# Performance work log

Measured on AMD Instinct MI355X. Metric: run time of the kernel, lower is better.

## Reference

```python
import jax, jax.numpy as jnp
import numpy as np

D, H, E, K, S = 1024, 2048, 8, 2, 1  # dim, expert hidden, n_experts, top_k, n_shared
B, L = 4, 2048


def setup_inputs() -> dict:
    key = jax.random.key(0)
    ks = jax.random.split(key, 9)
    std = 0.02
    return {
        "x": jax.random.normal(ks[0], (B, L, D), dtype=jnp.float32),
        "router_w": jax.random.normal(ks[1], (E, D), dtype=jnp.float32) * std,
        "experts_bias": jnp.zeros((E,), dtype=jnp.float32),  # aux-free LB bias buffer
        "w1": jax.random.normal(ks[2], (E, D, H), dtype=jnp.float32) * std,
        "w3": jax.random.normal(ks[3], (E, D, H), dtype=jnp.float32) * std,
        "w2": jax.random.normal(ks[4], (E, H, D), dtype=jnp.float32) * std,
        "sw1": jax.random.normal(ks[5], (S, D, H), dtype=jnp.float32) * std,
        "sw3": jax.random.normal(ks[6], (S, D, H), dtype=jnp.float32) * std,
        "sw2": jax.random.normal(ks[7], (S, H, D), dtype=jnp.float32) * std,
    }


def reference(x, router_w, experts_bias, w1, w3, w2, sw1, sw3, sw2):
    b, l, d = x.shape
    xf = x.reshape(-1, d)  # [T, D], T = b*l

    # shared experts (SwiGLU FFN), summed over S
    sg = jnp.einsum("td,sdh->tsh", xf, sw1)
    su = jnp.einsum("td,sdh->tsh", xf, sw3)
    shared_out = jnp.einsum("tsh,shd->td", jax.nn.silu(sg) * su, sw2)

    # router + aux-free load-balancing bias
    logits = xf @ router_w.T + experts_bias  # [T, E]
    rw, sel = jax.lax.top_k(logits, K)       # [T, K]
    rw = jax.nn.softmax(rw.astype(jnp.float32), axis=-1).astype(x.dtype)

    # combine weights scattered to [T, E]; equals torch one_hot dispatch+index_add
    cw = (jax.nn.one_hot(sel, E, dtype=x.dtype) * rw[..., None]).sum(axis=1)

    # all-expert SwiGLU, weighted-combined (identical math: unselected weight = 0)
    g = jnp.einsum("td,edh->teh", xf, w1)
    u = jnp.einsum("td,edh->teh", xf, w3)
    eo = jax.nn.silu(g) * u  # [T, E, H]
    moe_out = jnp.einsum("te,teh,ehd->td", cw, eo, w2)

    return (moe_out + shared_out).reshape(b, l, d)
```

## Files before the change

kernel.cpp:

```cpp
#include <hip/hip_runtime.h>
#include <stdint.h>

#define T_TOK 8192
#define DIMV  1024
#define HIDV  2048
#define NE    8
#define CAP   8192
#define ROUTED 16384
#define ASSIGN_TOT 24576

typedef __attribute__((ext_vector_type(8))) short          bf16x8;
typedef __attribute__((ext_vector_type(8))) unsigned short u16x8;
typedef __attribute__((ext_vector_type(4))) float          floatx4;

__device__ __forceinline__ unsigned short f2bf(float f) {
    union { float f; unsigned int i; } v; v.f = f;
    unsigned int i = v.i;
    return (unsigned short)((i + 0x7FFFu + ((i >> 16) & 1u)) >> 16);
}
__device__ __forceinline__ float bf2f(unsigned short u) {
    union { unsigned int i; float f; } v; v.i = ((unsigned int)u) << 16; return v.f;
}

__device__ __forceinline__ void gll16(const void* g, void* l) {
    __builtin_amdgcn_global_load_lds((const __attribute__((address_space(1))) void*)g,
                                     (__attribute__((address_space(3))) void*)l,
                                     16, 0, 0);
}

__global__ __launch_bounds__(256) void router_kernel(
    const float* __restrict__ x,
    const float* __restrict__ rwp,
    const float* __restrict__ biasp,
    unsigned short* __restrict__ xb,
    int* __restrict__ cnt, int* __restrict__ tlist,
    int* __restrict__ pos, float* __restrict__ pw)
{
    const int t    = blockIdx.x * 4 + (threadIdx.x >> 6);
    const int lane = threadIdx.x & 63;
    const float* xr = x + (size_t)t * DIMV + lane * 16;
    float xf[16];
#pragma unroll
    for (int q = 0; q < 4; q++) {
        float4 v = *(const float4*)(xr + q * 4);
        xf[q*4+0] = v.x; xf[q*4+1] = v.y; xf[q*4+2] = v.z; xf[q*4+3] = v.w;
    }
    {
        u16x8 o0, o1;
#pragma unroll
        for (int j = 0; j < 8; j++) { o0[j] = f2bf(xf[j]); o1[j] = f2bf(xf[8 + j]); }
        unsigned short* xo = xb + (size_t)t * DIMV + lane * 16;
        *(u16x8*)xo = o0;
        *(u16x8*)(xo + 8) = o1;
    }
    float acc[NE];
#pragma unroll
    for (int e = 0; e < NE; e++) {
        const float* wr = rwp + (size_t)e * DIMV + lane * 16;
        float s = 0.f;
#pragma unroll
        for (int q = 0; q < 4; q++) {
            float4 v = *(const float4*)(wr + q * 4);
            s += xf[q*4+0]*v.x + xf[q*4+1]*v.y + xf[q*4+2]*v.z + xf[q*4+3]*v.w;
        }
        acc[e] = s;
    }
#pragma unroll
    for (int e = 0; e < NE; e++)
#pragma unroll
        for (int off = 32; off; off >>= 1) acc[e] += __shfl_xor(acc[e], off, 64);

    if (lane == 0) {
        float lg[NE];
#pragma unroll
        for (int e = 0; e < NE; e++) lg[e] = acc[e] + biasp[e];
        int e0 = 0;
#pragma unroll
        for (int e = 1; e < NE; e++) if (lg[e] > lg[e0]) e0 = e;
        int e1 = (e0 == 0) ? 1 : 0;
#pragma unroll
        for (int e = 0; e < NE; e++) if (e != e0 && lg[e] > lg[e1]) e1 = e;
        float z  = __expf(lg[e1] - lg[e0]);
        float p0 = 1.f / (1.f + z);
        float p1 = z  / (1.f + z);
        int s0 = atomicAdd(cnt + e0, 1);
        tlist[e0 * CAP + s0] = t;
        int s1 = atomicAdd(cnt + e1, 1);
        tlist[e1 * CAP + s1] = t;
        pos[2 * t + 0] = e0 * CAP + s0;
        pos[2 * t + 1] = e1 * CAP + s1;
        pw[2 * t + 0] = p0;
        pw[2 * t + 1] = p1;
    }
}

template<int R, int C>
__device__ __forceinline__ void ctrans_body(
    const float* __restrict__ src, unsigned short* __restrict__ dstp,
    unsigned short (*tile)[66])
{
    const int c0 = blockIdx.x * 64, r0 = blockIdx.y * 64;
    const int tid = threadIdx.x;
    const int lr = tid >> 4;
    const int lc = (tid & 15) * 4;
#pragma unroll
    for (int i = 0; i < 4; i++) {
        int r = lr + 16 * i;
        float4 v = *(const float4*)(src + (size_t)(r0 + r) * C + (c0 + lc));
        ushort4 o; o.x = f2bf(v.x); o.y = f2bf(v.y); o.z = f2bf(v.z); o.w = f2bf(v.w);
        *(ushort4*)&tile[r][lc] = o;
    }
    __syncthreads();
    const int oc  = tid >> 3;
    const int orr = (tid & 7) * 8;
#pragma unroll
    for (int i = 0; i < 2; i++) {
        int c = oc + 32 * i;
        u16x8 tmp;
#pragma unroll
        for (int j = 0; j < 8; j++) tmp[j] = tile[orr + j][c];
        *(u16x8*)(dstp + (size_t)(c0 + c) * R + (r0 + orr)) = tmp;
    }
}

__global__ __launch_bounds__(256) void ctrans_all(
    const float* __restrict__ w1, const float* __restrict__ w3,
    const float* __restrict__ sw1, const float* __restrict__ sw3,
    const float* __restrict__ w2, const float* __restrict__ sw2,
    unsigned short* __restrict__ w1t, unsigned short* __restrict__ w3t,
    unsigned short* __restrict__ sw1t, unsigned short* __restrict__ sw3t,
    unsigned short* __restrict__ w2t, unsigned short* __restrict__ sw2t)
{
    __shared__ unsigned short tile[64][66];
    const int z = blockIdx.z;
    if (z < 18) {
        if (blockIdx.y >= DIMV / 64) return;
        const float* src; unsigned short* dstp;
        if (z < 8)        { src = w1 + (size_t)z * DIMV * HIDV;       dstp = w1t + (size_t)z * DIMV * HIDV; }
        else if (z < 16)  { src = w3 + (size_t)(z - 8) * DIMV * HIDV; dstp = w3t + (size_t)(z - 8) * DIMV * HIDV; }
        else if (z == 16) { src = sw1; dstp = sw1t; }
        else              { src = sw3; dstp = sw3t; }
        ctrans_body<DIMV, HIDV>(src, dstp, tile);
    } else {
        if (blockIdx.x >= DIMV / 64) return;
        const float* src; unsigned short* dstp;
        if (z < 26) { src = w2 + (size_t)(z - 18) * HIDV * DIMV; dstp = w2t + (size_t)(z - 18) * HIDV * DIMV; }
        else        { src = sw2; dstp = sw2t; }
        ctrans_body<HIDV, DIMV>(src, dstp, tile);
    }
}

__global__ __launch_bounds__(256, 2) void up_gemm(
    const unsigned short* __restrict__ x,
    const unsigned short* __restrict__ w1t,
    const unsigned short* __restrict__ w3t,
    const unsigned short* __restrict__ sw1t,
    const unsigned short* __restrict__ sw3t,
    const int* __restrict__ cnt, const int* __restrict__ tlist,
    unsigned short* __restrict__ hbuf)
{
    const int g = blockIdx.z;
    int n_rows, row_off;
    const unsigned short *B1p, *B3p;
    if (g < NE) {
        row_off = 0;
        for (int e = 0; e < g; e++) row_off += cnt[e];
        n_rows = cnt[g];
        B1p = w1t + (size_t)g * HIDV * DIMV;
        B3p = w3t + (size_t)g * HIDV * DIMV;
    } else {
        n_rows = T_TOK; row_off = ROUTED;
        B1p = sw1t; B3p = sw3t;
    }
    const int m0 = blockIdx.y * 128;
    if (m0 >= n_rows) return;
    const int n0 = blockIdx.x * 64;

    __shared__ __align__(16) unsigned short Al[128 * 32];
    __shared__ __align__(16) unsigned short B1l[64 * 32];
    __shared__ __align__(16) unsigned short B3l[64 * 32];

    const int tid  = threadIdx.x;
    const int lane = tid & 63;
    const int wave = tid >> 6;
    const int r0   = tid >> 2;
    const int ck   = (tid & 3) ^ ((r0 >> 1) & 3);

    int tokA, tokB;
    if (g < NE) {
        int ra = m0 + r0, rb = m0 + 64 + r0;
        tokA = (ra < n_rows) ? tlist[g * CAP + ra] : 0;
        tokB = (rb < n_rows) ? tlist[g * CAP + rb] : 0;
    } else { tokA = m0 + r0; tokB = m0 + 64 + r0; }

    const unsigned short* gA0 = x + (size_t)tokA * DIMV + ck * 8;
    const unsigned short* gA1 = x + (size_t)tokB * DIMV + ck * 8;
    const unsigned short* gB1 = B1p + (size_t)(n0 + r0) * DIMV + ck * 8;
    const unsigned short* gB3 = B3p + (size_t)(n0 + r0) * DIMV + ck * 8;

    char* AlB0 = (char*)Al  + wave * 1024;
    char* AlB1 = (char*)Al  + 4096 + wave * 1024;
    char* B1B  = (char*)B1l + wave * 1024;
    char* B3B  = (char*)B3l + wave * 1024;

    const int wm = wave & 1, wn = wave >> 1;
    const int m16 = lane & 15, quad = lane >> 4;
    const int sw  = (m16 >> 1) & 3;

    floatx4 accg[4][2] = {};
    floatx4 accu[4][2] = {};

    const unsigned short* Afp  = Al  + (wm * 64 + m16) * 32 + (quad ^ sw) * 8;
    const unsigned short* B1fp = B1l + (wn * 32 + m16) * 32 + (quad ^ sw) * 8;
    const unsigned short* B3fp = B3l + (wn * 32 + m16) * 32 + (quad ^ sw) * 8;

    for (int k0 = 0; k0 < DIMV; k0 += 32) {
        __syncthreads();
        gll16(gA0 + k0, AlB0);
        gll16(gA1 + k0, AlB1);
        gll16(gB1 + k0, B1B);
        gll16(gB3 + k0, B3B);
        __syncthreads();
        bf16x8 af[4], b1f[2], b3f[2];
#pragma unroll
        for (int i = 0; i < 4; i++) af[i] = *(const bf16x8*)(Afp + i * 16 * 32);
#pragma unroll
        for (int j = 0; j < 2; j++) {
            b1f[j] = *(const bf16x8*)(B1fp + j * 16 * 32);
            b3f[j] = *(const bf16x8*)(B3fp + j * 16 * 32);
        }
#pragma unroll
        for (int i = 0; i < 4; i++)
#pragma unroll
            for (int j = 0; j < 2; j++) {
                accg[i][j] = __builtin_amdgcn_mfma_f32_16x16x32_bf16(af[i], b1f[j], accg[i][j], 0, 0, 0);
                accu[i][j] = __builtin_amdgcn_mfma_f32_16x16x32_bf16(af[i], b3f[j], accu[i][j], 0, 0, 0);
            }
    }

#pragma unroll
    for (int i = 0; i < 4; i++) {
#pragma unroll
        for (int ii = 0; ii < 4; ii++) {
            int r = m0 + wm * 64 + i * 16 + quad * 4 + ii;
            if (r < n_rows) {
#pragma unroll
                for (int j = 0; j < 2; j++) {
                    int col = n0 + wn * 32 + j * 16 + m16;
                    float gv = accg[i][j][ii], uv = accu[i][j][ii];
                    float s  = gv / (1.0f + __expf(-gv));
                    hbuf[(size_t)(row_off + r) * HIDV + col] = f2bf(s * uv);
                }
            }
        }
    }
}

__global__ __launch_bounds__(256, 2) void down_gemm(
    const unsigned short* __restrict__ hbuf,
    const unsigned short* __restrict__ w2t,
    const unsigned short* __restrict__ sw2t,
    const int* __restrict__ cnt,
    unsigned short* __restrict__ dbuf)
{
    const int g = blockIdx.z;
    int n_rows, row_off;
    const unsigned short* Bp;
    if (g < NE) {
        row_off = 0;
        for (int e = 0; e < g; e++) row_off += cnt[e];
        n_rows = cnt[g];
        Bp = w2t + (size_t)g * DIMV * HIDV;
    } else {
        n_rows = T_TOK; row_off = ROUTED;
        Bp = sw2t;
    }
    const int m0 = blockIdx.y * 128;
    if (m0 >= n_rows) return;
    const int n0 = blockIdx.x * 128;

    __shared__ __align__(16) unsigned short Al[128 * 32];
    __shared__ __align__(16) unsigned short Bl[128 * 32];

    const int tid  = threadIdx.x;
    const int lane = tid & 63;
    const int wave = tid >> 6;
    const int r0   = tid >> 2;
    const int ck   = (tid & 3) ^ ((r0 >> 1) & 3);

    const unsigned short* gA0 = hbuf + (size_t)(row_off + m0 + r0) * HIDV + ck * 8;
    const unsigned short* gA1 = gA0 + (size_t)64 * HIDV;
    const unsigned short* gB0 = Bp + (size_t)(n0 + r0) * HIDV + ck * 8;
    const unsigned short* gB1 = gB0 + (size_t)64 * HIDV;

    char* AlB0 = (char*)Al + wave * 1024;
    char* AlB1 = (char*)Al + 4096 + wave * 1024;
    char* BB0  = (char*)Bl + wave * 1024;
    char* BB1  = (char*)Bl + 4096 + wave * 1024;

    const int wm = wave & 1, wn = wave >> 1;
    const int m16 = lane & 15, quad = lane >> 4;
    const int sw  = (m16 >> 1) & 3;

    floatx4 acc[4][4] = {};

    const unsigned short* Afp = Al + (wm * 64 + m16) * 32 + (quad ^ sw) * 8;
    const unsigned short* Bfp = Bl + (wn * 64 + m16) * 32 + (quad ^ sw) * 8;

    for (int k0 = 0; k0 < HIDV; k0 += 32) {
        __syncthreads();
        gll16(gA0 + k0, AlB0);
        gll16(gA1 + k0, AlB1);
        gll16(gB0 + k0, BB0);
        gll16(gB1 + k0, BB1);
        __syncthreads();
        bf16x8 af[4], bf[4];
#pragma unroll
        for (int i = 0; i < 4; i++) af[i] = *(const bf16x8*)(Afp + i * 16 * 32);
#pragma unroll
        for (int j = 0; j < 4; j++) bf[j] = *(const bf16x8*)(Bfp + j * 16 * 32);
#pragma unroll
        for (int i = 0; i < 4; i++)
#pragma unroll
            for (int j = 0; j < 4; j++)
                acc[i][j] = __builtin_amdgcn_mfma_f32_16x16x32_bf16(af[i], bf[j], acc[i][j], 0, 0, 0);
    }

#pragma unroll
    for (int i = 0; i < 4; i++) {
#pragma unroll
        for (int ii = 0; ii < 4; ii++) {
            int r = m0 + wm * 64 + i * 16 + quad * 4 + ii;
            if (r < n_rows) {
                unsigned short* drow = dbuf + (size_t)(row_off + r) * DIMV;
#pragma unroll
                for (int j = 0; j < 4; j++) {
                    int col = n0 + wn * 64 + j * 16 + m16;
                    drow[col] = f2bf(acc[i][j][ii]);
                }
            }
        }
    }
}

__global__ __launch_bounds__(256) void combine_kernel(
    const unsigned short* __restrict__ dbuf,
    const int* __restrict__ cnt, const int* __restrict__ pos,
    const float* __restrict__ pw, float* __restrict__ outp)
{
    const int tid = threadIdx.x;
    const int t = blockIdx.x * 2 + (tid >> 7);
    const int c = (tid & 127) * 8;
    int goff[NE];
    {
        int s = 0;
#pragma unroll
        for (int e = 0; e < NE; e++) { goff[e] = s; s += cnt[e]; }
    }
    const int p0 = pos[2 * t], p1 = pos[2 * t + 1];
    const float w0 = pw[2 * t], w1 = pw[2 * t + 1];
    const int r0 = goff[p0 >> 13] + (p0 & (CAP - 1));
    const int r1 = goff[p1 >> 13] + (p1 & (CAP - 1));
    const u16x8 v0 = *(const u16x8*)(dbuf + (size_t)r0 * DIMV + c);
    const u16x8 v1 = *(const u16x8*)(dbuf + (size_t)r1 * DIMV + c);
    const u16x8 vs = *(const u16x8*)(dbuf + (size_t)(ROUTED + t) * DIMV + c);
    float o[8];
#pragma unroll
    for (int j = 0; j < 8; j++)
        o[j] = w0 * bf2f(v0[j]) + w1 * bf2f(v1[j]) + bf2f(vs[j]);
    float* op = outp + (size_t)t * DIMV + c;
    *(float4*)op       = make_float4(o[0], o[1], o[2], o[3]);
    *(float4*)(op + 4) = make_float4(o[4], o[5], o[6], o[7]);
}

extern "C" void kernel_launch(void* const* d_in, const int* in_sizes, int n_in,
                              void* d_out, int out_size, void* d_ws, size_t ws_size,
                              hipStream_t stream)
{
    (void)in_sizes; (void)n_in; (void)out_size; (void)ws_size;
    const float* x    = (const float*)d_in[0];
    const float* rw   = (const float*)d_in[1];
    const float* bias = (const float*)d_in[2];
    const float* w1   = (const float*)d_in[3];
    const float* w3   = (const float*)d_in[4];
    const float* w2   = (const float*)d_in[5];
    const float* sw1  = (const float*)d_in[6];
    const float* sw3  = (const float*)d_in[7];
    const float* sw2  = (const float*)d_in[8];
    float* outp = (float*)d_out;

    char* p = (char*)d_ws;
    auto alloc = [&](size_t b) { char* r = p; p += (b + 255) & ~(size_t)255; return r; };
    int*   cnt   = (int*)  alloc(64);
    int*   tlist = (int*)  alloc((size_t)NE * CAP * 4);
    int*   pos   = (int*)  alloc((size_t)T_TOK * 2 * 4);
    float* pw    = (float*)alloc((size_t)T_TOK * 2 * 4);
    unsigned short* xb   = (unsigned short*)alloc((size_t)T_TOK * DIMV * 2);
    unsigned short* hbuf = (unsigned short*)alloc((size_t)ASSIGN_TOT * HIDV * 2);
    unsigned short* w1t  = (unsigned short*)alloc((size_t)NE * HIDV * DIMV * 2);
    unsigned short* w3t  = (unsigned short*)alloc((size_t)NE * HIDV * DIMV * 2);
    unsigned short* w2t  = (unsigned short*)alloc((size_t)NE * DIMV * HIDV * 2);
    unsigned short* sw1t = (unsigned short*)alloc((size_t)HIDV * DIMV * 2);
    unsigned short* sw3t = (unsigned short*)alloc((size_t)HIDV * DIMV * 2);
    unsigned short* sw2t = (unsigned short*)alloc((size_t)DIMV * HIDV * 2);
    unsigned short* dbuf = w1t;

    hipMemsetAsync(cnt, 0, 64, stream);

    dim3 blk(256);
    router_kernel<<<dim3(T_TOK/4), blk, 0, stream>>>(x, rw, bias, xb, cnt, tlist, pos, pw);
    ctrans_all<<<dim3(HIDV/64, HIDV/64, 27), blk, 0, stream>>>(w1, w3, sw1, sw3, w2, sw2,
                                                               w1t, w3t, sw1t, sw3t, w2t, sw2t);
    up_gemm<<<dim3(HIDV/64, 64, 9), blk, 0, stream>>>(xb, w1t, w3t, sw1t, sw3t,
                                                      cnt, tlist, hbuf);
    down_gemm<<<dim3(DIMV/128, 64, 9), blk, 0, stream>>>(hbuf, w2t, sw2t, cnt, dbuf);
    combine_kernel<<<dim3(T_TOK/2), blk, 0, stream>>>(dbuf, cnt, pos, pw, outp);
}
```

Measured before the change: 858.3 us.

## Rewrite up/down GEMMs as 256x256-tile, 8-wave, double-buffered pipelined kernels with interleaved w1/w3

The weight transpose now interleaves w1 and w3 rows in 16-row groups into one concatenated matrix, so the up GEMM becomes a single GEMM with gate/up pairs side by side. Both expert GEMMs move to 512-thread blocks with 256x256 output tiles and 128 KB dynamic LDS, double-buffered so global-to-LDS loads for upcoming k-steps overlap the MFMA work. The loop uses explicit waitcnt, barrier and setprio scheduling. This aims for more data reuse per LDS byte and better latency hiding. The cost is much larger tiles, which waste more work on partially filled expert tiles and allow fewer blocks per CU. Relying on 128 KB of dynamic shared memory also assumes the launch supports that size.

```diff
diff --git a/kernel.cpp b/kernel.cpp
--- a/kernel.cpp
+++ b/kernel.cpp
@@ -8,6 +8,7 @@
 #define CAP   8192
 #define ROUTED 16384
 #define ASSIGN_TOT 24576
+#define NCAT  4096
 
 typedef __attribute__((ext_vector_type(8))) short          bf16x8;
 typedef __attribute__((ext_vector_type(8))) unsigned short u16x8;
@@ -97,7 +98,7 @@
 template<int R, int C>
 __device__ __forceinline__ void ctrans_body(
     const float* __restrict__ src, unsigned short* __restrict__ dstp,
-    unsigned short (*tile)[66])
+    unsigned short (*tile)[66], int ileave, int ubit)
 {
     const int c0 = blockIdx.x * 64, r0 = blockIdx.y * 64;
     const int tid = threadIdx.x;
@@ -116,10 +117,12 @@
 #pragma unroll
     for (int i = 0; i < 2; i++) {
         int c = oc + 32 * i;
+        int h = c0 + c;
+        int row = ileave ? (((h >> 4) << 5) + ubit * 16 + (h & 15)) : h;
         u16x8 tmp;
 #pragma unroll
         for (int j = 0; j < 8; j++) tmp[j] = tile[orr + j][c];
-        *(u16x8*)(dstp + (size_t)(c0 + c) * R + (r0 + orr)) = tmp;
+        *(u16x8*)(dstp + (size_t)row * R + (r0 + orr)) = tmp;
     }
 }
 
@@ -127,136 +130,180 @@
     const float* __restrict__ w1, const float* __restrict__ w3,
     const float* __restrict__ sw1, const float* __restrict__ sw3,
     const float* __restrict__ w2, const float* __restrict__ sw2,
-    unsigned short* __restrict__ w1t, unsigned short* __restrict__ w3t,
-    unsigned short* __restrict__ sw1t, unsigned short* __restrict__ sw3t,
+    unsigned short* __restrict__ wcat, unsigned short* __restrict__ scat,
     unsigned short* __restrict__ w2t, unsigned short* __restrict__ sw2t)
 {
     __shared__ unsigned short tile[64][66];
     const int z = blockIdx.z;
     if (z < 18) {
         if (blockIdx.y >= DIMV / 64) return;
-        const float* src; unsigned short* dstp;
-        if (z < 8)        { src = w1 + (size_t)z * DIMV * HIDV;       dstp = w1t + (size_t)z * DIMV * HIDV; }
-        else if (z < 16)  { src = w3 + (size_t)(z - 8) * DIMV * HIDV; dstp = w3t + (size_t)(z - 8) * DIMV * HIDV; }
-        else if (z == 16) { src = sw1; dstp = sw1t; }
-        else              { src = sw3; dstp = sw3t; }
-        ctrans_body<DIMV, HIDV>(src, dstp, tile);
+        const float* src; unsigned short* dstp; int u;
+        if (z < 8)        { src = w1 + (size_t)z * DIMV * HIDV;       dstp = wcat + (size_t)z * NCAT * DIMV;       u = 0; }
+        else if (z < 16)  { src = w3 + (size_t)(z - 8) * DIMV * HIDV; dstp = wcat + (size_t)(z - 8) * NCAT * DIMV; u = 1; }
+        else if (z == 16) { src = sw1; dstp = scat; u = 0; }
+        else              { src = sw3; dstp = scat; u = 1; }
+        ctrans_body<DIMV, HIDV>(src, dstp, tile, 1, u);
     } else {
         if (blockIdx.x >= DIMV / 64) return;
         const float* src; unsigned short* dstp;
-        if (z < 26) { src = w2 + (size_t)(z - 18) * HIDV * DIMV; dstp = w2t + (size_t)(z - 18) * HIDV * DIMV; }
+        if (z < 26) { src = w2 + (size_t)(z - 18) * HIDV * DIMV; dstp = w2t + (size_t)(z - 18) * DIMV * HIDV; }
         else        { src = sw2; dstp = sw2t; }
-        ctrans_body<HIDV, DIMV>(src, dstp, tile);
-    }
-}
-
-__global__ __launch_bounds__(256, 2) void up_gemm(
+        ctrans_body<HIDV, DIMV>(src, dstp, tile, 0, 0);
+    }
+}
+
+
+__global__ __launch_bounds__(512, 2) void up_gemm8(
     const unsigned short* __restrict__ x,
-    const unsigned short* __restrict__ w1t,
-    const unsigned short* __restrict__ w3t,
-    const unsigned short* __restrict__ sw1t,
-    const unsigned short* __restrict__ sw3t,
+    const unsigned short* __restrict__ wcat,
+    const unsigned short* __restrict__ scat,
     const int* __restrict__ cnt, const int* __restrict__ tlist,
     unsigned short* __restrict__ hbuf)
 {
     const int g = blockIdx.z;
-    int n_rows, row_off;
-    const unsigned short *B1p, *B3p;
+    int n_rows, row_off = 0;
+    const unsigned short* Bp;
     if (g < NE) {
-        row_off = 0;
         for (int e = 0; e < g; e++) row_off += cnt[e];
         n_rows = cnt[g];
-        B1p = w1t + (size_t)g * HIDV * DIMV;
-        B3p = w3t + (size_t)g * HIDV * DIMV;
-    } else {
-        n_rows = T_TOK; row_off = ROUTED;
-        B1p = sw1t; B3p = sw3t;
-    }
-    const int m0 = blockIdx.y * 128;
+        Bp = wcat + (size_t)g * NCAT * DIMV;
+    } else { n_rows = T_TOK; row_off = ROUTED; Bp = scat; }
+    const int m0 = blockIdx.y * 256;
     if (m0 >= n_rows) return;
-    const int n0 = blockIdx.x * 64;
-
-    __shared__ __align__(16) unsigned short Al[128 * 32];
-    __shared__ __align__(16) unsigned short B1l[64 * 32];
-    __shared__ __align__(16) unsigned short B3l[64 * 32];
+    const int n0 = blockIdx.x * 256;
+
+    extern __shared__ __align__(16) unsigned short smem[];
+    unsigned short* As = smem;
+    unsigned short* Bs = smem + 32768;
 
     const int tid  = threadIdx.x;
     const int lane = tid & 63;
     const int wave = tid >> 6;
-    const int r0   = tid >> 2;
-    const int ck   = (tid & 3) ^ ((r0 >> 1) & 3);
-
-    int tokA, tokB;
+    const int wm = wave >> 2, wn = wave & 3;
+    const int m16 = lane & 15, quad = lane >> 4;
+
+    const int sr = tid >> 2;
+    const int sc = (((tid & 3) ^ (sr & 3)) << 3);
+
+    int tA0, tA1;
     if (g < NE) {
-        int ra = m0 + r0, rb = m0 + 64 + r0;
-        tokA = (ra < n_rows) ? tlist[g * CAP + ra] : 0;
-        tokB = (rb < n_rows) ? tlist[g * CAP + rb] : 0;
-    } else { tokA = m0 + r0; tokB = m0 + 64 + r0; }
-
-    const unsigned short* gA0 = x + (size_t)tokA * DIMV + ck * 8;
-    const unsigned short* gA1 = x + (size_t)tokB * DIMV + ck * 8;
-    const unsigned short* gB1 = B1p + (size_t)(n0 + r0) * DIMV + ck * 8;
-    const unsigned short* gB3 = B3p + (size_t)(n0 + r0) * DIMV + ck * 8;
-
-    char* AlB0 = (char*)Al  + wave * 1024;
-    char* AlB1 = (char*)Al  + 4096 + wave * 1024;
-    char* B1B  = (char*)B1l + wave * 1024;
-    char* B3B  = (char*)B3l + wave * 1024;
-
-    const int wm = wave & 1, wn = wave >> 1;
-    const int m16 = lane & 15, quad = lane >> 4;
-    const int sw  = (m16 >> 1) & 3;
-
-    floatx4 accg[4][2] = {};
-    floatx4 accu[4][2] = {};
-
-    const unsigned short* Afp  = Al  + (wm * 64 + m16) * 32 + (quad ^ sw) * 8;
-    const unsigned short* B1fp = B1l + (wn * 32 + m16) * 32 + (quad ^ sw) * 8;
-    const unsigned short* B3fp = B3l + (wn * 32 + m16) * 32 + (quad ^ sw) * 8;
-
-    for (int k0 = 0; k0 < DIMV; k0 += 32) {
-        __syncthreads();
-        gll16(gA0 + k0, AlB0);
-        gll16(gA1 + k0, AlB1);
-        gll16(gB1 + k0, B1B);
-        gll16(gB3 + k0, B3B);
-        __syncthreads();
-        bf16x8 af[4], b1f[2], b3f[2];
-#pragma unroll
-        for (int i = 0; i < 4; i++) af[i] = *(const bf16x8*)(Afp + i * 16 * 32);
-#pragma unroll
-        for (int j = 0; j < 2; j++) {
-            b1f[j] = *(const bf16x8*)(B1fp + j * 16 * 32);
-            b3f[j] = *(const bf16x8*)(B3fp + j * 16 * 32);
-        }
-#pragma unroll
-        for (int i = 0; i < 4; i++)
-#pragma unroll
-            for (int j = 0; j < 2; j++) {
-                accg[i][j] = __builtin_amdgcn_mfma_f32_16x16x32_bf16(af[i], b1f[j], accg[i][j], 0, 0, 0);
-                accu[i][j] = __builtin_amdgcn_mfma_f32_16x16x32_bf16(af[i], b3f[j], accu[i][j], 0, 0, 0);
-            }
-    }
-
-#pragma unroll
-    for (int i = 0; i < 4; i++) {
+        int ra = m0 + sr;       if (ra >= n_rows) ra = n_rows - 1;
+        int rb = m0 + 128 + sr; if (rb >= n_rows) rb = n_rows - 1;
+        tA0 = tlist[g * CAP + ra];
+        tA1 = tlist[g * CAP + rb];
+    } else { tA0 = m0 + sr; tA1 = m0 + 128 + sr; }
+    const unsigned short* sA0 = x + (size_t)tA0 * DIMV + sc;
+    const unsigned short* sA1 = x + (size_t)tA1 * DIMV + sc;
+    const unsigned short* sB0 = Bp + (size_t)(n0 + sr) * DIMV + sc;
+    const unsigned short* sB1 = Bp + (size_t)(n0 + 128 + sr) * DIMV + sc;
+
+    unsigned short* dA = As + wave * 512;
+    unsigned short* dB = Bs + wave * 512;
+
+#define UPSA(t, kk) { unsigned short* d_ = dA + (((t) & 1) << 14) + ((kk) << 13); \
+        gll16(sA0 + (t) * 64 + (kk) * 32, d_); gll16(sA1 + (t) * 64 + (kk) * 32, d_ + 4096); }
+#define UPSB(t, kk) { unsigned short* d_ = dB + (((t) & 1) << 14) + ((kk) << 13); \
+        gll16(sB0 + (t) * 64 + (kk) * 32, d_); gll16(sB1 + (t) * 64 + (kk) * 32, d_ + 4096); }
+
+    const unsigned short* Afb = As + (wm * 128 + m16) * 32 + ((quad ^ (m16 & 3)) << 3);
+    const unsigned short* Bfb = Bs + (wn * 64  + m16) * 32 + ((quad ^ (m16 & 3)) << 3);
+
+    UPSB(0, 0); UPSA(0, 0); UPSB(0, 1); UPSA(0, 1);
+    UPSB(1, 0); UPSA(1, 0); UPSB(1, 1);
+    asm volatile("s_waitcnt vmcnt(6)" ::: "memory");
+    __builtin_amdgcn_s_barrier();
+
+    floatx4 acc[8][4] = {};
+    bf16x8 af[4], bfr[4];
+
+#define NTU 16
+    for (int t = 0; t < NTU; ++t) {
+        const int pb = (t & 1) << 14;
+        const unsigned short* Ab = Afb + pb;
+        const unsigned short* Bb = Bfb + pb;
+#pragma unroll
+        for (int i = 0; i < 4; i++) af[i]  = *(const bf16x8*)(Ab + i * 512);
+#pragma unroll
+        for (int j = 0; j < 4; j++) bfr[j] = *(const bf16x8*)(Bb + j * 512);
+        if (t + 1 < NTU) UPSA(t + 1, 1);
+        __builtin_amdgcn_s_barrier();
+        asm volatile("s_waitcnt lgkmcnt(0)" ::: "memory");
+        __builtin_amdgcn_s_setprio(1);
+#pragma unroll
+        for (int i = 0; i < 4; i++)
+#pragma unroll
+            for (int j = 0; j < 4; j++)
+                acc[i][j] = __builtin_amdgcn_mfma_f32_16x16x32_bf16(af[i], bfr[j], acc[i][j], 0, 0, 0);
+        __builtin_amdgcn_s_setprio(0);
+        __builtin_amdgcn_s_barrier();
+#pragma unroll
+        for (int i = 0; i < 4; i++) af[i] = *(const bf16x8*)(Ab + (4 + i) * 512);
+        if (t + 2 < NTU) UPSB(t + 2, 0);
+        __builtin_amdgcn_s_barrier();
+        asm volatile("s_waitcnt lgkmcnt(0)" ::: "memory");
+        __builtin_amdgcn_s_setprio(1);
+#pragma unroll
+        for (int i = 0; i < 4; i++)
+#pragma unroll
+            for (int j = 0; j < 4; j++)
+                acc[4 + i][j] = __builtin_amdgcn_mfma_f32_16x16x32_bf16(af[i], bfr[j], acc[4 + i][j], 0, 0, 0);
+        __builtin_amdgcn_s_setprio(0);
+        __builtin_amdgcn_s_barrier();
+#pragma unroll
+        for (int i = 0; i < 4; i++) af[i]  = *(const bf16x8*)(Ab + 8192 + i * 512);
+#pragma unroll
+        for (int j = 0; j < 4; j++) bfr[j] = *(const bf16x8*)(Bb + 8192 + j * 512);
+        if (t + 2 < NTU) UPSA(t + 2, 0);
+        __builtin_amdgcn_s_barrier();
+        asm volatile("s_waitcnt lgkmcnt(0)" ::: "memory");
+        __builtin_amdgcn_s_setprio(1);
+#pragma unroll
+        for (int i = 0; i < 4; i++)
+#pragma unroll
+            for (int j = 0; j < 4; j++)
+                acc[i][j] = __builtin_amdgcn_mfma_f32_16x16x32_bf16(af[i], bfr[j], acc[i][j], 0, 0, 0);
+        __builtin_amdgcn_s_setprio(0);
+        __builtin_amdgcn_s_barrier();
+#pragma unroll
+        for (int i = 0; i < 4; i++) af[i] = *(const bf16x8*)(Ab + 8192 + (4 + i) * 512);
+        if (t + 2 < NTU) UPSB(t + 2, 1);
+        __builtin_amdgcn_s_barrier();
+        asm volatile("s_waitcnt lgkmcnt(0)" ::: "memory");
+        __builtin_amdgcn_s_setprio(1);
+#pragma unroll
+        for (int i = 0; i < 4; i++)
+#pragma unroll
+            for (int j = 0; j < 4; j++)
+                acc[4 + i][j] = __builtin_amdgcn_mfma_f32_16x16x32_bf16(af[i], bfr[j], acc[4 + i][j], 0, 0, 0);
+        __builtin_amdgcn_s_setprio(0);
+        if (t < NTU - 2) { asm volatile("s_waitcnt vmcnt(6)" ::: "memory"); }
+        else             { asm volatile("s_waitcnt vmcnt(0)" ::: "memory"); }
+        __builtin_amdgcn_s_barrier();
+    }
+#undef NTU
+#undef UPSA
+#undef UPSB
+
+    const int hb = (n0 >> 1) + wn * 32;
+#pragma unroll
+    for (int mi = 0; mi < 8; mi++) {
 #pragma unroll
         for (int ii = 0; ii < 4; ii++) {
-            int r = m0 + wm * 64 + i * 16 + quad * 4 + ii;
+            int r = m0 + wm * 128 + mi * 16 + quad * 4 + ii;
             if (r < n_rows) {
-#pragma unroll
-                for (int j = 0; j < 2; j++) {
-                    int col = n0 + wn * 32 + j * 16 + m16;
-                    float gv = accg[i][j][ii], uv = accu[i][j][ii];
+                unsigned short* hr = hbuf + (size_t)(row_off + r) * HIDV;
+#pragma unroll
+                for (int p = 0; p < 2; p++) {
+                    float gv = acc[mi][2 * p][ii], uv = acc[mi][2 * p + 1][ii];
                     float s  = gv / (1.0f + __expf(-gv));
-                    hbuf[(size_t)(row_off + r) * HIDV + col] = f2bf(s * uv);
+                    hr[hb + p * 16 + m16] = f2bf(s * uv);
                 }
             }
         }
     }
 }
 
-__global__ __launch_bounds__(256, 2) void down_gemm(
+__global__ __launch_bounds__(512, 2) void down_gemm8(
     const unsigned short* __restrict__ hbuf,
     const unsigned short* __restrict__ w2t,
     const unsigned short* __restrict__ sw2t,
@@ -264,80 +311,132 @@
     unsigned short* __restrict__ dbuf)
 {
     const int g = blockIdx.z;
-    int n_rows, row_off;
+    int n_rows, row_off = 0;
     const unsigned short* Bp;
     if (g < NE) {
-        row_off = 0;
         for (int e = 0; e < g; e++) row_off += cnt[e];
         n_rows = cnt[g];
         Bp = w2t + (size_t)g * DIMV * HIDV;
-    } else {
-        n_rows = T_TOK; row_off = ROUTED;
-        Bp = sw2t;
-    }
-    const int m0 = blockIdx.y * 128;
+    } else { n_rows = T_TOK; row_off = ROUTED; Bp = sw2t; }
+    const int m0 = blockIdx.y * 256;
     if (m0 >= n_rows) return;
-    const int n0 = blockIdx.x * 128;
-
-    __shared__ __align__(16) unsigned short Al[128 * 32];
-    __shared__ __align__(16) unsigned short Bl[128 * 32];
+    const int n0 = blockIdx.x * 256;
+
+    extern __shared__ __align__(16) unsigned short smem[];
+    unsigned short* As = smem;
+    unsigned short* Bs = smem + 32768;
 
     const int tid  = threadIdx.x;
     const int lane = tid & 63;
     const int wave = tid >> 6;
-    const int r0   = tid >> 2;
-    const int ck   = (tid & 3) ^ ((r0 >> 1) & 3);
-
-    const unsigned short* gA0 = hbuf + (size_t)(row_off + m0 + r0) * HIDV + ck * 8;
-    const unsigned short* gA1 = gA0 + (size_t)64 * HIDV;
-    const unsigned short* gB0 = Bp + (size_t)(n0 + r0) * HIDV + ck * 8;
-    const unsigned short* gB1 = gB0 + (size_t)64 * HIDV;
-
-    char* AlB0 = (char*)Al + wave * 1024;
-    char* AlB1 = (char*)Al + 4096 + wave * 1024;
-    char* BB0  = (char*)Bl + wave * 1024;
-    char* BB1  = (char*)Bl + 4096 + wave * 1024;
-
-    const int wm = wave & 1, wn = wave >> 1;
+    const int wm = wave >> 2, wn = wave & 3;
     const int m16 = lane & 15, quad = lane >> 4;
-    const int sw  = (m16 >> 1) & 3;
-
-    floatx4 acc[4][4] = {};
-
-    const unsigned short* Afp = Al + (wm * 64 + m16) * 32 + (quad ^ sw) * 8;
-    const unsigned short* Bfp = Bl + (wn * 64 + m16) * 32 + (quad ^ sw) * 8;
-
-    for (int k0 = 0; k0 < HIDV; k0 += 32) {
-        __syncthreads();
-        gll16(gA0 + k0, AlB0);
-        gll16(gA1 + k0, AlB1);
-        gll16(gB0 + k0, BB0);
-        gll16(gB1 + k0, BB1);
-        __syncthreads();
-        bf16x8 af[4], bf[4];
-#pragma unroll
-        for (int i = 0; i < 4; i++) af[i] = *(const bf16x8*)(Afp + i * 16 * 32);
-#pragma unroll
-        for (int j = 0; j < 4; j++) bf[j] = *(const bf16x8*)(Bfp + j * 16 * 32);
-#pragma unroll
-        for (int i = 0; i < 4; i++)
-#pragma unroll
-            for (int j = 0; j < 4; j++)
-                acc[i][j] = __builtin_amdgcn_mfma_f32_16x16x32_bf16(af[i], bf[j], acc[i][j], 0, 0, 0);
-    }
-
-#pragma unroll
-    for (int i = 0; i < 4; i++) {
+
+    const int sr = tid >> 2;
+    const int sc = (((tid & 3) ^ (sr & 3)) << 3);
+
+    const unsigned short* sA0 = hbuf + (size_t)(row_off + m0 + sr) * HIDV + sc;
+    const unsigned short* sA1 = sA0 + (size_t)128 * HIDV;
+    const unsigned short* sB0 = Bp + (size_t)(n0 + sr) * HIDV + sc;
+    const unsigned short* sB1 = sB0 + (size_t)128 * HIDV;
+
+    unsigned short* dA = As + wave * 512;
+    unsigned short* dB = Bs + wave * 512;
+
+#define DNSA(t, kk) { unsigned short* d_ = dA + (((t) & 1) << 14) + ((kk) << 13); \
+        gll16(sA0 + (t) * 64 + (kk) * 32, d_); gll16(sA1 + (t) * 64 + (kk) * 32, d_ + 4096); }
+#define DNSB(t, kk) { unsigned short* d_ = dB + (((t) & 1) << 14) + ((kk) << 13); \
+        gll16(sB0 + (t) * 64 + (kk) * 32, d_); gll16(sB1 + (t) * 64 + (kk) * 32, d_ + 4096); }
+
+    const unsigned short* Afb = As + (wm * 128 + m16) * 32 + ((quad ^ (m16 & 3)) << 3);
+    const unsigned short* Bfb = Bs + (wn * 64  + m16) * 32 + ((quad ^ (m16 & 3)) << 3);
+
+    DNSB(0, 0); DNSA(0, 0); DNSB(0, 1); DNSA(0, 1);
+    DNSB(1, 0); DNSA(1, 0); DNSB(1, 1);
+    asm volatile("s_waitcnt vmcnt(6)" ::: "memory");
+    __builtin_amdgcn_s_barrier();
+
+    floatx4 acc[8][4] = {};
+    bf16x8 af[4], bfr[4];
+
+#define NTD 32
+    for (int t = 0; t < NTD; ++t) {
+        const int pb = (t & 1) << 14;
+        const unsigned short* Ab = Afb + pb;
+        const unsigned short* Bb = Bfb + pb;
+#pragma unroll
+        for (int i = 0; i < 4; i++) af[i]  = *(const bf16x8*)(Ab + i * 512);
+#pragma unroll
+        for (int j = 0; j < 4; j++) bfr[j] = *(const bf16x8*)(Bb + j * 512);
+        if (t + 1 < NTD) DNSA(t + 1, 1);
+        __builtin_amdgcn_s_barrier();
+        asm volatile("s_waitcnt lgkmcnt(0)" ::: "memory");
+        __builtin_amdgcn_s_setprio(1);
+#pragma unroll
+        for (int i = 0; i < 4; i++)
+#pragma unroll
+            for (int j = 0; j < 4; j++)
+                acc[i][j] = __builtin_amdgcn_mfma_f32_16x16x32_bf16(af[i], bfr[j], acc[i][j], 0, 0, 0);
+        __builtin_amdgcn_s_setprio(0);
+        __builtin_amdgcn_s_barrier();
+#pragma unroll
+        for (int i = 0; i < 4; i++) af[i] = *(const bf16x8*)(Ab + (4 + i) * 512);
+        if (t + 2 < NTD) DNSB(t + 2, 0);
+        __builtin_amdgcn_s_barrier();
+        asm volatile("s_waitcnt lgkmcnt(0)" ::: "memory");
+        __builtin_amdgcn_s_setprio(1);
+#pragma unroll
+        for (int i = 0; i < 4; i++)
+#pragma unroll
+            for (int j = 0; j < 4; j++)
+                acc[4 + i][j] = __builtin_amdgcn_mfma_f32_16x16x32_bf16(af[i], bfr[j], acc[4 + i][j], 0, 0, 0);
+        __builtin_amdgcn_s_setprio(0);
+        __builtin_amdgcn_s_barrier();
+#pragma unroll
+        for (int i = 0; i < 4; i++) af[i]  = *(const bf16x8*)(Ab + 8192 + i * 512);
+#pragma unroll
+        for (int j = 0; j < 4; j++) bfr[j] = *(const bf16x8*)(Bb + 8192 + j * 512);
+        if (t + 2 < NTD) DNSA(t + 2, 0);
+        __builtin_amdgcn_s_barrier();
+        asm volatile("s_waitcnt lgkmcnt(0)" ::: "memory");
+        __builtin_amdgcn_s_setprio(1);
+#pragma unroll
+        for (int i = 0; i < 4; i++)
+#pragma unroll
+            for (int j = 0; j < 4; j++)
+                acc[i][j] = __builtin_amdgcn_mfma_f32_16x16x32_bf16(af[i], bfr[j], acc[i][j], 0, 0, 0);
+        __builtin_amdgcn_s_setprio(0);
+        __builtin_amdgcn_s_barrier();
+#pragma unroll
+        for (int i = 0; i < 4; i++) af[i] = *(const bf16x8*)(Ab + 8192 + (4 + i) * 512);
+        if (t + 2 < NTD) DNSB(t + 2, 1);
+        __builtin_amdgcn_s_barrier();
+        asm volatile("s_waitcnt lgkmcnt(0)" ::: "memory");
+        __builtin_amdgcn_s_setprio(1);
+#pragma unroll
+        for (int i = 0; i < 4; i++)
+#pragma unroll
+            for (int j = 0; j < 4; j++)
+                acc[4 + i][j] = __builtin_amdgcn_mfma_f32_16x16x32_bf16(af[i], bfr[j], acc[4 + i][j], 0, 0, 0);
+        __builtin_amdgcn_s_setprio(0);
+        if (t < NTD - 2) { asm volatile("s_waitcnt vmcnt(6)" ::: "memory"); }
+        else             { asm volatile("s_waitcnt vmcnt(0)" ::: "memory"); }
+        __builtin_amdgcn_s_barrier();
+    }
+#undef NTD
+#undef DNSA
+#undef DNSB
+
+#pragma unroll
+    for (int mi = 0; mi < 8; mi++) {
 #pragma unroll
         for (int ii = 0; ii < 4; ii++) {
-            int r = m0 + wm * 64 + i * 16 + quad * 4 + ii;
+            int r = m0 + wm * 128 + mi * 16 + quad * 4 + ii;
             if (r < n_rows) {
                 unsigned short* drow = dbuf + (size_t)(row_off + r) * DIMV;
 #pragma unroll
-                for (int j = 0; j < 4; j++) {
-                    int col = n0 + wn * 64 + j * 16 + m16;
-                    drow[col] = f2bf(acc[i][j][ii]);
-                }
+                for (int nj = 0; nj < 4; nj++)
+                    drow[n0 + wn * 64 + nj * 16 + m16] = f2bf(acc[mi][nj][ii]);
             }
         }
     }
@@ -397,22 +496,21 @@
     float* pw    = (float*)alloc((size_t)T_TOK * 2 * 4);
     unsigned short* xb   = (unsigned short*)alloc((size_t)T_TOK * DIMV * 2);
     unsigned short* hbuf = (unsigned short*)alloc((size_t)ASSIGN_TOT * HIDV * 2);
-    unsigned short* w1t  = (unsigned short*)alloc((size_t)NE * HIDV * DIMV * 2);
-    unsigned short* w3t  = (unsigned short*)alloc((size_t)NE * HIDV * DIMV * 2);
+    unsigned short* wcat = (unsigned short*)alloc((size_t)NE * NCAT * DIMV * 2);
+    unsigned short* scat = (unsigned short*)alloc((size_t)NCAT * DIMV * 2);
     unsigned short* w2t  = (unsigned short*)alloc((size_t)NE * DIMV * HIDV * 2);
-    unsigned short* sw1t = (unsigned short*)alloc((size_t)HIDV * DIMV * 2);
-    unsigned short* sw3t = (unsigned short*)alloc((size_t)HIDV * DIMV * 2);
     unsigned short* sw2t = (unsigned short*)alloc((size_t)DIMV * HIDV * 2);
-    unsigned short* dbuf = w1t;
+    unsigned short* dbuf = wcat;
 
     hipMemsetAsync(cnt, 0, 64, stream);
 
     dim3 blk(256);
     router_kernel<<<dim3(T_TOK/4), blk, 0, stream>>>(x, rw, bias, xb, cnt, tlist, pos, pw);
     ctrans_all<<<dim3(HIDV/64, HIDV/64, 27), blk, 0, stream>>>(w1, w3, sw1, sw3, w2, sw2,
-                                                               w1t, w3t, sw1t, sw3t, w2t, sw2t);
-    up_gemm<<<dim3(HIDV/64, 64, 9), blk, 0, stream>>>(xb, w1t, w3t, sw1t, sw3t,
-                                                      cnt, tlist, hbuf);
-    down_gemm<<<dim3(DIMV/128, 64, 9), blk, 0, stream>>>(hbuf, w2t, sw2t, cnt, dbuf);
+                                                               wcat, scat, w2t, sw2t);
+    up_gemm8<<<dim3(NCAT/256, 32, 9), dim3(512), 131072, stream>>>(xb, wcat, scat,
+                                                                   cnt, tlist, hbuf);
+    down_gemm8<<<dim3(DIMV/256, 32, 9), dim3(512), 131072, stream>>>(hbuf, w2t, sw2t,
+                                                                     cnt, dbuf);
     combine_kernel<<<dim3(T_TOK/2), blk, 0, stream>>>(dbuf, cnt, pos, pw, outp);
 }
```

Result: faster. 819.8 us (-4.5%).
